# Performance work log

Hardware: AMD Instinct MI355X
Metric: run time of the kernel (lower is better)

The kernel has to match this reference:

```python
import jax, jax.numpy as jnp
import numpy as np

N_NODES = 20000
N_EDGES = 240000
IN_DIM = 20
SH_DIM = 16  # (lmax+1)^2 with lmax=3
DENOM = 1.0
EPS = 1e-12


def spherical_harmonics_lmax3(v):
    """Real spherical harmonics l=0..3 on unit vectors v: [E,3] -> [E,16]."""
    x, y, z = v[:, 0], v[:, 1], v[:, 2]
    x2, y2, z2 = x * x, y * y, z * z
    sh = [
        jnp.full_like(x, 0.28209479177387814),            # l=0
        0.4886025119029199 * y,                            # l=1, m=-1
        0.4886025119029199 * z,                            # l=1, m=0
        0.4886025119029199 * x,                            # l=1, m=1
        1.0925484305920792 * x * y,                        # l=2, m=-2
        1.0925484305920792 * y * z,                        # l=2, m=-1
        0.31539156525252005 * (3.0 * z2 - 1.0),            # l=2, m=0
        1.0925484305920792 * x * z,                        # l=2, m=1
        0.5462742152960396 * (x2 - y2),                    # l=2, m=2
        0.5900435899266435 * y * (3.0 * x2 - y2),          # l=3, m=-3
        2.890611442640554 * x * y * z,                     # l=3, m=-2
        0.4570457994644658 * y * (5.0 * z2 - 1.0),         # l=3, m=-1
        0.3731763325901154 * z * (5.0 * z2 - 3.0),         # l=3, m=0
        0.4570457994644658 * x * (5.0 * z2 - 1.0),         # l=3, m=1
        1.445305721320277 * z * (x2 - y2),                 # l=3, m=2
        0.5900435899266435 * x * (x2 - 3.0 * y2),          # l=3, m=3
    ]
    return jnp.stack(sh, axis=-1)


def setup_inputs() -> dict:
    key = jax.random.key(0)
    ks = jax.random.split(key, 10)
    x = jax.random.normal(ks[0], (N_NODES, IN_DIM), dtype=jnp.float32)
    positions = jax.random.normal(ks[1], (N_NODES, 3), dtype=jnp.float32)
    edge_index = jax.random.randint(ks[2], (2, N_EDGES), 0, N_NODES, dtype=jnp.int32)
    s = 1.0 / np.sqrt(IN_DIM)
    W_pre = jax.random.uniform(ks[3], (IN_DIM, IN_DIM), jnp.float32, -s, s)
    b_pre = jax.random.uniform(ks[4], (IN_DIM,), jnp.float32, -s, s)
    W_post = jax.random.uniform(ks[5], (IN_DIM, IN_DIM), jnp.float32, -s, s)
    b_post = jax.random.uniform(ks[6], (IN_DIM,), jnp.float32, -s, s)
    W_sc = jax.random.uniform(ks[7], (IN_DIM, IN_DIM), jnp.float32, -s, s)
    b_sc = jax.random.uniform(ks[8], (IN_DIM,), jnp.float32, -s, s)
    return {"x": x, "positions": positions, "edge_index": edge_index,
            "W_pre": W_pre, "b_pre": b_pre, "W_post": W_post, "b_post": b_post,
            "W_sc": W_sc, "b_sc": b_sc}


def reference(x, positions, edge_index, W_pre, b_pre, W_post, b_post, W_sc, b_sc):
    row, col = edge_index[0], edge_index[1]
    # per-edge gather + relative positions
    rel = positions[col] - positions[row]                      # [E,3]
    norm = jnp.sqrt(jnp.sum(rel * rel, axis=-1, keepdims=True) + EPS)
    sh = spherical_harmonics_lmax3(rel / norm)                 # [E,16]
    sender = x[row]                                            # [E,20]
    # equivariant tensor product (outer product over irreps channels)
    tp = (sender[:, :, None] * sh[:, None, :]).reshape(sender.shape[0], IN_DIM * SH_DIM)  # [E,320]
    edge_features = jnp.concatenate([sender, tp], axis=1)      # [E,340]
    # scatter-add aggregation to target nodes
    aggr = jax.ops.segment_sum(edge_features, col, num_segments=N_NODES)  # [N,340]
    # node update MLP + shortcut (math of Layer.update)
    h = x / DENOM
    h = jax.nn.relu(h @ W_pre.T + b_pre)
    h = h @ W_post.T + b_post
    out = x @ W_sc.T + b_sc + h                                # [N,20]
    # aggr is computed (and aggregated) by the original propagate; concat so it stays live
    return jnp.concatenate([out, aggr], axis=1)                # [N,360]
```

## Files before the change

### kernel.cpp

```cpp
#include <hip/hip_runtime.h>

#define N_NODES 20000
#define N_EDGES 240000
#define IN_DIM  20
#define AGG_DIM 340
#define OUT_DIM 360
#define EPS_F   1e-12f
#define CAP     64
#define EDGE_BLOCKS ((N_EDGES + 255) / 256)
#define MLP_BLOCKS  ((N_NODES + 255) / 256)

typedef _Float16 half8 __attribute__((ext_vector_type(8)));

__device__ __forceinline__ float sh_coeff(int k, float xn, float yn, float zn) {
    const float x2 = xn * xn, y2 = yn * yn, z2 = zn * zn;
    switch (k) {
        case 0:  return 0.28209479177387814f;
        case 1:  return 0.4886025119029199f * yn;
        case 2:  return 0.4886025119029199f * zn;
        case 3:  return 0.4886025119029199f * xn;
        case 4:  return 1.0925484305920792f * xn * yn;
        case 5:  return 1.0925484305920792f * yn * zn;
        case 6:  return 0.31539156525252005f * (3.0f * z2 - 1.0f);
        case 7:  return 1.0925484305920792f * xn * zn;
        case 8:  return 0.5462742152960396f * (x2 - y2);
        case 9:  return 0.5900435899266435f * yn * (3.0f * x2 - y2);
        case 10: return 2.890611442640554f  * xn * yn * zn;
        case 11: return 0.4570457994644658f * yn * (5.0f * z2 - 1.0f);
        case 12: return 0.3731763325901154f * zn * (5.0f * z2 - 3.0f);
        case 13: return 0.4570457994644658f * xn * (5.0f * z2 - 1.0f);
        case 14: return 1.445305721320277f  * zn * (x2 - y2);
        default: return 0.5900435899266435f * xn * (x2 - 3.0f * y2);
    }
}

__global__ __launch_bounds__(256) void bucket_sh_mlp(
    const float* __restrict__ pos,
    const int* __restrict__ ei,
    const float* __restrict__ x,
    const float* __restrict__ Wpre,  const float* __restrict__ bpre,
    const float* __restrict__ Wpost, const float* __restrict__ bpost,
    const float* __restrict__ Wsc,   const float* __restrict__ bsc,
    int* __restrict__ counts,
    int* __restrict__ ovf_cnt,
    int* __restrict__ ovf,
    int* __restrict__ bucket,
    half8* __restrict__ shbuf,
    float* __restrict__ out)
{
    if ((int)blockIdx.x < EDGE_BLOCKS) {
        const int e = (int)(blockIdx.x * 256 + threadIdx.x);
        if (e >= N_EDGES) return;
        const int row = ei[e];
        const int col = ei[N_EDGES + e];
        const int slot = atomicAdd(&counts[col], 1);
        if (slot >= CAP) { ovf[atomicAdd(ovf_cnt, 1)] = e; return; }

        const int sidx = col * CAP + slot;
        bucket[sidx] = row;

        const float rx = pos[col * 3 + 0] - pos[row * 3 + 0];
        const float ry = pos[col * 3 + 1] - pos[row * 3 + 1];
        const float rz = pos[col * 3 + 2] - pos[row * 3 + 2];
        const float rinv = rsqrtf(rx * rx + ry * ry + rz * rz + EPS_F);
        const float xx = rx * rinv, yy = ry * rinv, zz = rz * rinv;
        const float x2 = xx * xx, y2 = yy * yy, z2 = zz * zz;

        const float sh0  = 0.28209479177387814f;
        const float sh1  = 0.4886025119029199f * yy;
        const float sh2  = 0.4886025119029199f * zz;
        const float sh3  = 0.4886025119029199f * xx;
        const float sh4  = 1.0925484305920792f * xx * yy;
        const float sh5  = 1.0925484305920792f * yy * zz;
        const float sh6  = 0.31539156525252005f * (3.0f * z2 - 1.0f);
        const float sh7  = 1.0925484305920792f * xx * zz;
        const float sh8  = 0.5462742152960396f * (x2 - y2);
        const float sh9  = 0.5900435899266435f * yy * (3.0f * x2 - y2);
        const float sh10 = 2.890611442640554f  * xx * yy * zz;
        const float sh11 = 0.4570457994644658f * yy * (5.0f * z2 - 1.0f);
        const float sh12 = 0.3731763325901154f * zz * (5.0f * z2 - 3.0f);
        const float sh13 = 0.4570457994644658f * xx * (5.0f * z2 - 1.0f);
        const float sh14 = 1.445305721320277f  * zz * (x2 - y2);
        const float sh15 = 0.5900435899266435f * xx * (x2 - 3.0f * y2);

        const half8 v0 = { (_Float16)sh12, (_Float16)sh13, (_Float16)sh14, (_Float16)sh15,
                           (_Float16)sh0,  (_Float16)sh1,  (_Float16)sh2,  (_Float16)sh3 };
        const half8 v1 = { (_Float16)sh4,  (_Float16)sh5,  (_Float16)sh6,  (_Float16)sh7,
                           (_Float16)sh8,  (_Float16)sh9,  (_Float16)sh10, (_Float16)sh11 };
        half8* dst = shbuf + (size_t)sidx * 2;
        dst[0] = v0;
        dst[1] = v1;
        return;
    }

    __shared__ float sWpre[IN_DIM * IN_DIM];
    __shared__ float sWpost[IN_DIM * IN_DIM];
    __shared__ float sWsc[IN_DIM * IN_DIM];
    __shared__ float sb[3 * IN_DIM];

    for (int t = threadIdx.x; t < IN_DIM * IN_DIM; t += 256) {
        sWpre[t]  = Wpre[t];
        sWpost[t] = Wpost[t];
        sWsc[t]   = Wsc[t];
    }
    if (threadIdx.x < IN_DIM) {
        sb[threadIdx.x]              = bpre[threadIdx.x];
        sb[IN_DIM + threadIdx.x]     = bpost[threadIdx.x];
        sb[2 * IN_DIM + threadIdx.x] = bsc[threadIdx.x];
    }
    __syncthreads();

    const int i = (int)((blockIdx.x - EDGE_BLOCKS) * 256 + threadIdx.x);
    if (i >= N_NODES) return;

    float xi[IN_DIM], h[IN_DIM];
#pragma unroll
    for (int j = 0; j < IN_DIM; ++j) xi[j] = x[(size_t)i * IN_DIM + j];

#pragma unroll
    for (int j = 0; j < IN_DIM; ++j) {
        float a = sb[j];
#pragma unroll
        for (int kk = 0; kk < IN_DIM; ++kk) a = fmaf(xi[kk], sWpre[j * IN_DIM + kk], a);
        h[j] = fmaxf(a, 0.0f);
    }
#pragma unroll
    for (int j = 0; j < IN_DIM; ++j) {
        float a = sb[IN_DIM + j] + sb[2 * IN_DIM + j];
#pragma unroll
        for (int kk = 0; kk < IN_DIM; ++kk) {
            a = fmaf(h[kk],  sWpost[j * IN_DIM + kk], a);
            a = fmaf(xi[kk], sWsc[j * IN_DIM + kk],  a);
        }
        out[(size_t)i * OUT_DIM + j] = a;
    }
}

__global__ __launch_bounds__(256) void node_gather(
    const float* __restrict__ x,
    const float* __restrict__ pos,
    const int* __restrict__ ei,
    const int* __restrict__ counts,
    const int* __restrict__ bucket,
    const _Float16* __restrict__ shbuf,
    const int* __restrict__ ovf_cnt,
    const int* __restrict__ ovf,
    float* __restrict__ out)
{
    const int lane   = threadIdx.x & 63;
    const int node   = (int)((blockIdx.x * blockDim.x + threadIdx.x) >> 6);
    const int lane20 = min(lane, IN_DIM - 1);
    const int lane16 = lane & 15;

    const int j0 = (lane >= IN_DIM) ? ((lane - IN_DIM) >> 4) : 0;
    const int j1 = (lane + 44)  >> 4;
    const int j2 = (lane + 108) >> 4;
    const int j3 = (lane + 172) >> 4;
    const int j4 = (lane + 236) >> 4;
    const int j5 = (lane + 300) >> 4;

    const int cnt_raw = __builtin_amdgcn_readfirstlane(counts[node]);
    const int cnt = min(cnt_raw, CAP);

    float acc0 = 0.f, acc1 = 0.f, acc2 = 0.f, acc3 = 0.f, acc4 = 0.f, acc5 = 0.f;
    float sum_s = 0.f;

#define ACCUM(S, SH)                                      \
    do {                                                  \
        sum_s += (S);                                     \
        acc0 = fmaf(__shfl((S), j0, 64), (SH), acc0);     \
        acc1 = fmaf(__shfl((S), j1, 64), (SH), acc1);     \
        acc2 = fmaf(__shfl((S), j2, 64), (SH), acc2);     \
        acc3 = fmaf(__shfl((S), j3, 64), (SH), acc3);     \
        acc4 = fmaf(__shfl((S), j4, 64), (SH), acc4);     \
        acc5 = fmaf(__shfl((S), j5, 64), (SH), acc5);     \
    } while (0)

    if (cnt > 0) {
        const int rl = bucket[node * CAP + min(lane, cnt - 1)];
        const _Float16* shb = shbuf + (size_t)node * CAP * 16 + lane16;

#define LOADCHUNK(B, S0, S1, S2, S3, H0, H1, H2, H3)                      \
    do {                                                                  \
        const int q1 = min((B) + 1, cnt - 1);                             \
        const int q2 = min((B) + 2, cnt - 1);                             \
        const int q3 = min((B) + 3, cnt - 1);                             \
        const int r0 = __builtin_amdgcn_readlane(rl, (B));                \
        const int r1 = __builtin_amdgcn_readlane(rl, q1);                 \
        const int r2 = __builtin_amdgcn_readlane(rl, q2);                 \
        const int r3 = __builtin_amdgcn_readlane(rl, q3);                 \
        S0 = x[(size_t)r0 * IN_DIM + lane20];                             \
        S1 = x[(size_t)r1 * IN_DIM + lane20];                             \
        S2 = x[(size_t)r2 * IN_DIM + lane20];                             \
        S3 = x[(size_t)r3 * IN_DIM + lane20];                             \
        H0 = (float)shb[(size_t)(B) * 16];                                \
        H1 = (float)shb[(size_t)q1 * 16];                                 \
        H2 = (float)shb[(size_t)q2 * 16];                                 \
        H3 = (float)shb[(size_t)q3 * 16];                                 \
    } while (0)

        float sA, sB, sC, sD, shA, shB, shC, shD;
        float tA, tB, tC, tD, uA, uB, uC, uD;

        LOADCHUNK(0, sA, sB, sC, sD, shA, shB, shC, shD);

        for (int base = 0; base < cnt; base += 4) {
            const int nb = base + 4;
            const bool have_next = nb < cnt;
            if (have_next)
                LOADCHUNK(nb, tA, tB, tC, tD, uA, uB, uC, uD);

            const float mB = (base + 1 < cnt) ? sB : 0.0f;
            const float mC = (base + 2 < cnt) ? sC : 0.0f;
            const float mD = (base + 3 < cnt) ? sD : 0.0f;

            ACCUM(sA, shA);
            ACCUM(mB, shB);
            ACCUM(mC, shC);
            ACCUM(mD, shD);

            if (have_next) {
                sA = tA; sB = tB; sC = tC; sD = tD;
                shA = uA; shB = uB; shC = uC; shD = uD;
            }
        }
#undef LOADCHUNK
    }

    if (cnt_raw > CAP) {
        const int m = *ovf_cnt;
        const int k = (lane + 12) & 15;
        for (int i = 0; i < m; ++i) {
            const int e = ovf[i];
            if (ei[N_EDGES + e] != node) continue;
            const int row = ei[e];
            const float rx = pos[node * 3 + 0] - pos[row * 3 + 0];
            const float ry = pos[node * 3 + 1] - pos[row * 3 + 1];
            const float rz = pos[node * 3 + 2] - pos[row * 3 + 2];
            const float rinv = rsqrtf(rx * rx + ry * ry + rz * rz + EPS_F);
            const float shk = sh_coeff(k, rx * rinv, ry * rinv, rz * rinv);
            const float s = x[(size_t)row * IN_DIM + lane20];
            ACCUM(s, shk);
        }
    }
#undef ACCUM

    float* obase = out + (size_t)node * OUT_DIM + IN_DIM;
    obase[lane]       = (lane < IN_DIM) ? sum_s : acc0;
    obase[lane + 64]  = acc1;
    obase[lane + 128] = acc2;
    obase[lane + 192] = acc3;
    obase[lane + 256] = acc4;
    if (lane < IN_DIM) obase[lane + 320] = acc5;
}

extern "C" void kernel_launch(void* const* d_in, const int* in_sizes, int n_in,
                              void* d_out, int out_size, void* d_ws, size_t ws_size,
                              hipStream_t stream)
{
    const float* x     = (const float*)d_in[0];
    const float* pos   = (const float*)d_in[1];
    const int*   ei    = (const int*)d_in[2];
    const float* Wpre  = (const float*)d_in[3];
    const float* bpre  = (const float*)d_in[4];
    const float* Wpost = (const float*)d_in[5];
    const float* bpost = (const float*)d_in[6];
    const float* Wsc   = (const float*)d_in[7];
    const float* bsc   = (const float*)d_in[8];
    float* out = (float*)d_out;

    half8* shbuf = (half8*)d_ws;
    int* ws_i    = (int*)((char*)d_ws + (size_t)N_NODES * CAP * 16 * sizeof(_Float16));
    int* counts  = ws_i;
    int* ovf_cnt = ws_i + N_NODES;
    int* ovf     = ws_i + N_NODES + 1;
    int* bucket  = ws_i + N_NODES + 1 + N_EDGES;

    hipMemsetAsync(counts, 0, (size_t)(N_NODES + 1) * sizeof(int), stream);

    bucket_sh_mlp<<<EDGE_BLOCKS + MLP_BLOCKS, 256, 0, stream>>>(
        pos, ei, x, Wpre, bpre, Wpost, bpost, Wsc, bsc,
        counts, ovf_cnt, ovf, bucket, shbuf, out);

    node_gather<<<(N_NODES * 64) / 256, 256, 0, stream>>>(
        x, pos, ei, counts, bucket, (const _Float16*)shbuf, ovf_cnt, ovf, out);
}
```

Baseline: 128.7 us.

## Compute per-node outer-product aggregation with MFMA using split-fp16 sender features

The per-node gather loop is replaced by 32x32x16 fp16 MFMA calls. They treat the aggregation as a [20 x k] by [k x 17] matrix product over the node's incoming edges, with an extra all-ones column that produces the plain sender sum. To keep accuracy, x is split into hi and lo fp16 halves (precomputed in the MLP branch into a packed workspace) and two MFMAs are accumulated. SH values are stored in a K-blocked packed layout so they can be loaded as B fragments. This removes the many shuffles and scalar FMAs per edge. In exchange it wastes MFMA lanes on padding and adds an extra x-pair write pass and masking logic.

```diff
diff --git a/kernel.cpp b/kernel.cpp
--- a/kernel.cpp
+++ b/kernel.cpp
@@ -1,16 +1,35 @@
 #include <hip/hip_runtime.h>
+#include <stdint.h>
 
 #define N_NODES 20000
 #define N_EDGES 240000
 #define IN_DIM  20
-#define AGG_DIM 340
 #define OUT_DIM 360
 #define EPS_F   1e-12f
 #define CAP     64
 #define EDGE_BLOCKS ((N_EDGES + 255) / 256)
 #define MLP_BLOCKS  ((N_NODES + 255) / 256)
 
-typedef _Float16 half8 __attribute__((ext_vector_type(8)));
+typedef _Float16 half8   __attribute__((ext_vector_type(8)));
+typedef float    floatx16 __attribute__((ext_vector_type(16)));
+typedef uint32_t uint4v  __attribute__((ext_vector_type(4)));
+
+__device__ __forceinline__ uint32_t pack_h2(float a, float b) {
+    union { _Float16 f[2]; uint32_t u; } t;
+    t.f[0] = (_Float16)a; t.f[1] = (_Float16)b;
+    return t.u;
+}
+
+__device__ __forceinline__ half8 h8_from_u32(uint32_t u0, uint32_t u1,
+                                             uint32_t u2, uint32_t u3) {
+    union { uint32_t u[4]; half8 h; } t;
+    t.u[0] = u0; t.u[1] = u1; t.u[2] = u2; t.u[3] = u3;
+    return t.h;
+}
+
+__device__ __forceinline__ uint32_t maskpair(int t, int j) {
+    return (t > j ? 0xFFFFu : 0u) | (t > j + 1 ? 0xFFFF0000u : 0u);
+}
 
 __device__ __forceinline__ float sh_coeff(int k, float xn, float yn, float zn) {
     const float x2 = xn * xn, y2 = yn * yn, z2 = zn * zn;
@@ -45,7 +64,8 @@
     int* __restrict__ ovf_cnt,
     int* __restrict__ ovf,
     int* __restrict__ bucket,
-    half8* __restrict__ shbuf,
+    uint32_t* __restrict__ shB,
+    uint32_t* __restrict__ xpair,
     float* __restrict__ out)
 {
     if ((int)blockIdx.x < EDGE_BLOCKS) {
@@ -56,8 +76,7 @@
         const int slot = atomicAdd(&counts[col], 1);
         if (slot >= CAP) { ovf[atomicAdd(ovf_cnt, 1)] = e; return; }
 
-        const int sidx = col * CAP + slot;
-        bucket[sidx] = row;
+        bucket[col * CAP + slot] = row;
 
         const float rx = pos[col * 3 + 0] - pos[row * 3 + 0];
         const float ry = pos[col * 3 + 1] - pos[row * 3 + 1];
@@ -83,13 +102,16 @@
         const float sh14 = 1.445305721320277f  * zz * (x2 - y2);
         const float sh15 = 0.5900435899266435f * xx * (x2 - 3.0f * y2);
 
-        const half8 v0 = { (_Float16)sh12, (_Float16)sh13, (_Float16)sh14, (_Float16)sh15,
-                           (_Float16)sh0,  (_Float16)sh1,  (_Float16)sh2,  (_Float16)sh3 };
-        const half8 v1 = { (_Float16)sh4,  (_Float16)sh5,  (_Float16)sh6,  (_Float16)sh7,
-                           (_Float16)sh8,  (_Float16)sh9,  (_Float16)sh10, (_Float16)sh11 };
-        half8* dst = shbuf + (size_t)sidx * 2;
-        dst[0] = v0;
-        dst[1] = v1;
+        const int bb = slot >> 4, kk = slot & 15;
+        uint32_t* dst = shB + (size_t)(col * 4 + bb) * 128 + kk;
+        dst[0 * 16] = pack_h2(sh0,  sh1);
+        dst[1 * 16] = pack_h2(sh2,  sh3);
+        dst[2 * 16] = pack_h2(sh4,  sh5);
+        dst[3 * 16] = pack_h2(sh6,  sh7);
+        dst[4 * 16] = pack_h2(sh8,  sh9);
+        dst[5 * 16] = pack_h2(sh10, sh11);
+        dst[6 * 16] = pack_h2(sh12, sh13);
+        dst[7 * 16] = pack_h2(sh14, sh15);
         return;
     }
 
@@ -116,6 +138,16 @@
     float xi[IN_DIM], h[IN_DIM];
 #pragma unroll
     for (int j = 0; j < IN_DIM; ++j) xi[j] = x[(size_t)i * IN_DIM + j];
+
+#pragma unroll
+    for (int j = 0; j < IN_DIM; ++j) {
+        const float v = xi[j];
+        const _Float16 hh = (_Float16)v;
+        const float res = v - (float)hh;
+        union { _Float16 f[2]; uint32_t u; } t;
+        t.f[0] = hh; t.f[1] = (_Float16)res;
+        xpair[(size_t)i * IN_DIM + j] = t.u;
+    }
 
 #pragma unroll
     for (int j = 0; j < IN_DIM; ++j) {
@@ -142,116 +174,118 @@
     const int* __restrict__ ei,
     const int* __restrict__ counts,
     const int* __restrict__ bucket,
-    const _Float16* __restrict__ shbuf,
+    const uint32_t* __restrict__ shB,
+    const uint32_t* __restrict__ xpair,
     const int* __restrict__ ovf_cnt,
     const int* __restrict__ ovf,
     float* __restrict__ out)
 {
-    const int lane   = threadIdx.x & 63;
-    const int node   = (int)((blockIdx.x * blockDim.x + threadIdx.x) >> 6);
-    const int lane20 = min(lane, IN_DIM - 1);
-    const int lane16 = lane & 15;
-
-    const int j0 = (lane >= IN_DIM) ? ((lane - IN_DIM) >> 4) : 0;
-    const int j1 = (lane + 44)  >> 4;
-    const int j2 = (lane + 108) >> 4;
-    const int j3 = (lane + 172) >> 4;
-    const int j4 = (lane + 236) >> 4;
-    const int j5 = (lane + 300) >> 4;
+    const int lane  = threadIdx.x & 63;
+    const int node  = (int)((blockIdx.x * blockDim.x + threadIdx.x) >> 6);
+    const int col   = lane & 31;
+    const int hi    = lane >> 5;
+    const int khalf = hi * 8;
+    const int rowc  = min(col, IN_DIM - 1);
 
     const int cnt_raw = __builtin_amdgcn_readfirstlane(counts[node]);
     const int cnt = min(cnt_raw, CAP);
 
-    float acc0 = 0.f, acc1 = 0.f, acc2 = 0.f, acc3 = 0.f, acc4 = 0.f, acc5 = 0.f;
-    float sum_s = 0.f;
-
-#define ACCUM(S, SH)                                      \
-    do {                                                  \
-        sum_s += (S);                                     \
-        acc0 = fmaf(__shfl((S), j0, 64), (SH), acc0);     \
-        acc1 = fmaf(__shfl((S), j1, 64), (SH), acc1);     \
-        acc2 = fmaf(__shfl((S), j2, 64), (SH), acc2);     \
-        acc3 = fmaf(__shfl((S), j3, 64), (SH), acc3);     \
-        acc4 = fmaf(__shfl((S), j4, 64), (SH), acc4);     \
-        acc5 = fmaf(__shfl((S), j5, 64), (SH), acc5);     \
-    } while (0)
+    floatx16 acc = {0,0,0,0,0,0,0,0,0,0,0,0,0,0,0,0};
 
     if (cnt > 0) {
-        const int rl = bucket[node * CAP + min(lane, cnt - 1)];
-        const _Float16* shb = shbuf + (size_t)node * CAP * 16 + lane16;
-
-#define LOADCHUNK(B, S0, S1, S2, S3, H0, H1, H2, H3)                      \
-    do {                                                                  \
-        const int q1 = min((B) + 1, cnt - 1);                             \
-        const int q2 = min((B) + 2, cnt - 1);                             \
-        const int q3 = min((B) + 3, cnt - 1);                             \
-        const int r0 = __builtin_amdgcn_readlane(rl, (B));                \
-        const int r1 = __builtin_amdgcn_readlane(rl, q1);                 \
-        const int r2 = __builtin_amdgcn_readlane(rl, q2);                 \
-        const int r3 = __builtin_amdgcn_readlane(rl, q3);                 \
-        S0 = x[(size_t)r0 * IN_DIM + lane20];                             \
-        S1 = x[(size_t)r1 * IN_DIM + lane20];                             \
-        S2 = x[(size_t)r2 * IN_DIM + lane20];                             \
-        S3 = x[(size_t)r3 * IN_DIM + lane20];                             \
-        H0 = (float)shb[(size_t)(B) * 16];                                \
-        H1 = (float)shb[(size_t)q1 * 16];                                 \
-        H2 = (float)shb[(size_t)q2 * 16];                                 \
-        H3 = (float)shb[(size_t)q3 * 16];                                 \
-    } while (0)
-
-        float sA, sB, sC, sD, shA, shB, shC, shD;
-        float tA, tB, tC, tD, uA, uB, uC, uD;
-
-        LOADCHUNK(0, sA, sB, sC, sD, shA, shB, shC, shD);
-
-        for (int base = 0; base < cnt; base += 4) {
-            const int nb = base + 4;
-            const bool have_next = nb < cnt;
-            if (have_next)
-                LOADCHUNK(nb, tA, tB, tC, tD, uA, uB, uC, uD);
-
-            const float mB = (base + 1 < cnt) ? sB : 0.0f;
-            const float mC = (base + 2 < cnt) ? sC : 0.0f;
-            const float mD = (base + 3 < cnt) ? sD : 0.0f;
-
-            ACCUM(sA, shA);
-            ACCUM(mB, shB);
-            ACCUM(mC, shC);
-            ACCUM(mD, shD);
-
-            if (have_next) {
-                sA = tA; sB = tB; sC = tC; sD = tD;
-                shA = uA; shB = uB; shC = uC; shD = uD;
-            }
-        }
-#undef LOADCHUNK
+        const int rl = bucket[node * CAP + lane];
+        const int nb = (cnt + 15) >> 4;
+        const uint32_t sel = (col & 1) ? 0x07060302u : 0x05040100u;
+
+        for (int b = 0; b < nb; ++b) {
+            const int sbase = 16 * b + khalf;
+
+            int rr[8];
+#pragma unroll
+            for (int j = 0; j < 8; ++j) {
+                int r = __shfl(rl, sbase + j, 64);
+                rr[j] = (int)min((uint32_t)r, (uint32_t)(N_NODES - 1));
+            }
+            uint32_t ee[8];
+#pragma unroll
+            for (int j = 0; j < 8; ++j)
+                ee[j] = xpair[(size_t)rr[j] * IN_DIM + rowc];
+
+            uint32_t a1u[4], a2u[4];
+#pragma unroll
+            for (int p = 0; p < 4; ++p) {
+                a1u[p] = (ee[2 * p] & 0xFFFFu)  | (ee[2 * p + 1] << 16);
+                a2u[p] = (ee[2 * p] >> 16)      | (ee[2 * p + 1] & 0xFFFF0000u);
+            }
+
+            uint32_t B0, B1, B2, B3;
+            if (col < 16) {
+                const uint32_t* bp = shB + ((size_t)(node * 4 + b) * 8 + (col >> 1)) * 16 + khalf;
+                const uint4v lo = *(const uint4v*)bp;
+                const uint4v hi4 = *(const uint4v*)(bp + 4);
+                B0 = __builtin_amdgcn_perm(lo[1],  lo[0],  sel);
+                B1 = __builtin_amdgcn_perm(lo[3],  lo[2],  sel);
+                B2 = __builtin_amdgcn_perm(hi4[1], hi4[0], sel);
+                B3 = __builtin_amdgcn_perm(hi4[3], hi4[2], sel);
+            } else if (col == 16) {
+                B0 = B1 = B2 = B3 = 0x3C003C00u;
+            } else {
+                B0 = B1 = B2 = B3 = 0u;
+            }
+            const int rem = cnt - 16 * b;
+            if (rem < 16) {
+                const int t = rem - khalf;
+                B0 &= maskpair(t, 0);
+                B1 &= maskpair(t, 2);
+                B2 &= maskpair(t, 4);
+                B3 &= maskpair(t, 6);
+            }
+
+            const half8 hb  = h8_from_u32(B0, B1, B2, B3);
+            const half8 ha1 = h8_from_u32(a1u[0], a1u[1], a1u[2], a1u[3]);
+            const half8 ha2 = h8_from_u32(a2u[0], a2u[1], a2u[2], a2u[3]);
+            acc = __builtin_amdgcn_mfma_f32_32x32x16_f16(ha1, hb, acc, 0, 0, 0);
+            acc = __builtin_amdgcn_mfma_f32_32x32x16_f16(ha2, hb, acc, 0, 0, 0);
+        }
     }
 
     if (cnt_raw > CAP) {
         const int m = *ovf_cnt;
-        const int k = (lane + 12) & 15;
-        for (int i = 0; i < m; ++i) {
-            const int e = ovf[i];
+        for (int t2 = 0; t2 < m; ++t2) {
+            const int e = ovf[t2];
             if (ei[N_EDGES + e] != node) continue;
             const int row = ei[e];
             const float rx = pos[node * 3 + 0] - pos[row * 3 + 0];
             const float ry = pos[node * 3 + 1] - pos[row * 3 + 1];
             const float rz = pos[node * 3 + 2] - pos[row * 3 + 2];
             const float rinv = rsqrtf(rx * rx + ry * ry + rz * rz + EPS_F);
-            const float shk = sh_coeff(k, rx * rinv, ry * rinv, rz * rinv);
-            const float s = x[(size_t)row * IN_DIM + lane20];
-            ACCUM(s, shk);
-        }
-    }
-#undef ACCUM
-
-    float* obase = out + (size_t)node * OUT_DIM + IN_DIM;
-    obase[lane]       = (lane < IN_DIM) ? sum_s : acc0;
-    obase[lane + 64]  = acc1;
-    obase[lane + 128] = acc2;
-    obase[lane + 192] = acc3;
-    obase[lane + 256] = acc4;
-    if (lane < IN_DIM) obase[lane + 320] = acc5;
+            float shc;
+            if (col < 16)      shc = sh_coeff(col, rx * rinv, ry * rinv, rz * rinv);
+            else if (col == 16) shc = 1.0f;
+            else                shc = 0.0f;
+#pragma unroll
+            for (int r = 0; r < 16; ++r) {
+                const int rw = ((r & 3) + 8 * (r >> 2)) + 4 * hi;
+                if (rw < IN_DIM)
+                    acc[r] = fmaf(x[(size_t)row * IN_DIM + rw], shc, acc[r]);
+            }
+        }
+    }
+
+    float* orow = out + (size_t)node * OUT_DIM;
+    if (col < 16) {
+#pragma unroll
+        for (int r = 0; r < 16; ++r) {
+            const int rw = ((r & 3) + 8 * (r >> 2)) + 4 * hi;
+            if (rw < IN_DIM) orow[2 * IN_DIM + rw * 16 + col] = acc[r];
+        }
+    } else if (col == 16) {
+#pragma unroll
+        for (int r = 0; r < 16; ++r) {
+            const int rw = ((r & 3) + 8 * (r >> 2)) + 4 * hi;
+            if (rw < IN_DIM) orow[IN_DIM + rw] = acc[r];
+        }
+    }
 }
 
 extern "C" void kernel_launch(void* const* d_in, const int* in_sizes, int n_in,
@@ -269,8 +303,9 @@
     const float* bsc   = (const float*)d_in[8];
     float* out = (float*)d_out;
 
-    half8* shbuf = (half8*)d_ws;
-    int* ws_i    = (int*)((char*)d_ws + (size_t)N_NODES * CAP * 16 * sizeof(_Float16));
+    uint32_t* shB   = (uint32_t*)d_ws;
+    uint32_t* xpair = shB + (size_t)N_NODES * 4 * 8 * 16;
+    int* ws_i    = (int*)(xpair + (size_t)N_NODES * IN_DIM);
     int* counts  = ws_i;
     int* ovf_cnt = ws_i + N_NODES;
     int* ovf     = ws_i + N_NODES + 1;
@@ -280,8 +315,8 @@
 
     bucket_sh_mlp<<<EDGE_BLOCKS + MLP_BLOCKS, 256, 0, stream>>>(
         pos, ei, x, Wpre, bpre, Wpost, bpost, Wsc, bsc,
-        counts, ovf_cnt, ovf, bucket, shbuf, out);
+        counts, ovf_cnt, ovf, bucket, shB, xpair, out);
 
     node_gather<<<(N_NODES * 64) / 256, 256, 0, stream>>>(
-        x, pos, ei, counts, bucket, (const _Float16*)shbuf, ovf_cnt, ovf, out);
-}
+        x, pos, ei, counts, bucket, shB, xpair, ovf_cnt, ovf, out);
+}
```

Result: slower. 132.5 us (+2.9%).
